# Optimization experiments

Hardware: AMD Instinct MI355X
Metric: run time of the kernel (lower is better)

## Reference

```python
import jax, jax.numpy as jnp
import numpy as np

B, N, E = 2, 16384, 262144          # batch, nodes, directed edges (avg deg 16)
K, D, Wm = 256, 3, 1                # nmodes, ndims, nmeasures
C, L, FC = 128, 4, 128              # channels, Fourier layers, fc hidden
IN_DIM, OUT_DIM = 3, 1


def setup_inputs() -> dict:
    key = jax.random.key(0)
    ks = jax.random.split(key, 20)
    s = 1.0 / (C * C)
    inp = {
        "x": jax.random.normal(ks[0], (B, N, IN_DIM), jnp.float32),
        "nodes": jax.random.uniform(ks[1], (B, N, D), jnp.float32),
        "node_mask": jnp.ones((B, N, 1), jnp.float32),
        "node_weights": jax.random.uniform(ks[2], (B, N, Wm), jnp.float32) / N,
        "directed_edges": jax.random.randint(ks[3], (B, E, 2), 0, N),
        "edge_gradient_weights": jax.random.normal(ks[4], (B, E, D), jnp.float32),
        "modes": jax.random.normal(ks[5], (K, D, Wm), jnp.float32),
        "sp_L": jnp.ones((D, Wm), jnp.float32),
        "weights_c": s * jax.random.uniform(ks[6], (L, C, C, K, Wm), jnp.float32),
        "weights_s": s * jax.random.uniform(ks[7], (L, C, C, K, Wm), jnp.float32),
        "weights_0": s * jax.random.uniform(ks[8], (L, C, C, 1, Wm), jnp.float32),
        "fc0_w": jax.random.normal(ks[9], (C, IN_DIM), jnp.float32) * 0.1,
        "fc0_b": jnp.zeros((C,), jnp.float32),
        "ws_w": jax.random.normal(ks[10], (L, C, C), jnp.float32) * 0.05,
        "ws_b": jnp.zeros((L, C), jnp.float32),
        "gws_w": jax.random.normal(ks[11], (L, C, D * C), jnp.float32) * 0.05,
        "gws_b": jnp.zeros((L, C), jnp.float32),
        "fc1_w": jax.random.normal(ks[12], (FC, C), jnp.float32) * 0.05,
        "fc1_b": jnp.zeros((FC,), jnp.float32),
        "fc2_w": jax.random.normal(ks[13], (OUT_DIM, FC), jnp.float32) * 0.05,
        "fc2_b": jnp.zeros((OUT_DIM,), jnp.float32),
    }
    return inp


def _gelu(x):
    return jax.nn.gelu(x, approximate=False)  # torch F.gelu default = exact erf


def _compute_gradient(f, directed_edges, edge_gradient_weights):
    # f: [B, C, N] -> gradients [B, C*D, N] via directed-edge scatter-add
    fT = jnp.transpose(f, (0, 2, 1))                       # [B, N, C]
    tgt, src = directed_edges[..., 0], directed_edges[..., 1]
    f_src = jnp.take_along_axis(fT, src[..., None], axis=1)  # [B, E, C]
    f_tgt = jnp.take_along_axis(fT, tgt[..., None], axis=1)
    msg = jnp.einsum('bed,bec->becd', edge_gradient_weights, f_src - f_tgt)
    msg = msg.reshape(msg.shape[0], msg.shape[1], -1)        # [B, E, C*D]

    def scat(m, t):
        return jnp.zeros((fT.shape[1], m.shape[-1]), m.dtype).at[t].add(m)

    g = jax.vmap(scat)(msg, tgt)                             # [B, N, C*D]
    return jnp.transpose(g, (0, 2, 1))


def _spectral_conv(x, wc, wsn, w0, bc, bs, b0, wbc, wbs, wb0):
    # x: [B, C_in, N]
    xc = jnp.einsum('bix,bxkw->bikw', x, wbc)
    xs = -jnp.einsum('bix,bxkw->bikw', x, wbs)
    x0 = jnp.einsum('bix,bxkw->bikw', x, wb0)
    fc = jnp.einsum('bikw,iokw->bokw', xc, wc) - jnp.einsum('bikw,iokw->bokw', xs, wsn)
    fs = jnp.einsum('bikw,iokw->bokw', xs, wc) + jnp.einsum('bikw,iokw->bokw', xc, wsn)
    f0 = jnp.einsum('bikw,iokw->bokw', x0, w0)
    return (jnp.einsum('bokw,bxkw->box', f0, b0)
            + 2.0 * jnp.einsum('bokw,bxkw->box', fc, bc)
            - 2.0 * jnp.einsum('bokw,bxkw->box', fs, bs))


def reference(x, nodes, node_mask, node_weights, directed_edges, edge_gradient_weights,
              modes, sp_L, weights_c, weights_s, weights_0,
              fc0_w, fc0_b, ws_w, ws_b, gws_w, gws_b, fc1_w, fc1_b, fc2_w, fc2_b):
    # Fourier bases with learnable length-scale sp_L: [K,D,Wm]*[D,Wm]
    temp = jnp.einsum('bxd,kdw->bxkw', nodes, modes * sp_L)   # [B,N,K,Wm]
    bc, bs = jnp.cos(temp), jnp.sin(temp)
    b0 = jnp.zeros((temp.shape[0], temp.shape[1], 1, temp.shape[3]), temp.dtype)
    nw = (node_weights * node_mask)[:, :, None, :]            # [B,N,1,Wm]
    wbc, wbs, wb0 = bc * nw, bs * nw, b0 * nw

    h = jnp.einsum('bxi,ci->bxc', x, fc0_w) + fc0_b           # lift [B,N,C]
    h = jnp.transpose(h, (0, 2, 1))                           # [B,C,N]

    for i in range(L):
        x1 = _spectral_conv(h, weights_c[i], weights_s[i], weights_0[i],
                            bc, bs, b0, wbc, wbs, wb0)
        x2 = jnp.einsum('oc,bcn->bon', ws_w[i], h) + ws_b[i][None, :, None]
        grad = _compute_gradient(h, directed_edges, edge_gradient_weights)
        x3 = jnp.einsum('og,bgn->bon', gws_w[i], grad) + gws_b[i][None, :, None]
        h = x1 + x2 + x3
        if i != L - 1:
            h = _gelu(h)

    h = jnp.transpose(h, (0, 2, 1))                           # [B,N,C]
    h = _gelu(jnp.einsum('bnc,fc->bnf', h, fc1_w) + fc1_b)
    out = jnp.einsum('bnf,of->bno', h, fc2_w) + fc2_b         # [B,N,out_dim]
    return out
```

## Files before the change

kernel.cpp:

```cpp
#include <hip/hip_runtime.h>
#include <math.h>

#define Bn 2
#define Nn 16384
#define En 262144
#define Kn 256
#define Cn 128
#define Rn 512
#define Ln 4
#define LDP 72
#define NSPLIT 64

typedef float f32x4 __attribute__((ext_vector_type(4)));
typedef short s16x8 __attribute__((ext_vector_type(8)));

__device__ __forceinline__ float gelu_f(float x){
  return 0.5f*x*(1.0f + erff(x*0.70710678118654752440f));
}
__device__ __forceinline__ unsigned short f2b(float x){
  unsigned int u = __float_as_uint(x);
  unsigned int r = (u + 0x7FFFu + ((u>>16)&1u)) >> 16;
  return (unsigned short)r;
}
__device__ __forceinline__ float b2f(unsigned short h){
  return __uint_as_float(((unsigned int)h)<<16);
}
__device__ __forceinline__ unsigned int pack2(float lo, float hi){
  return (unsigned int)f2b(lo) | ((unsigned int)f2b(hi) << 16);
}


__global__ __launch_bounds__(256) void k_nw(const float* __restrict__ nwt,
                                            const float* __restrict__ msk,
                                            float* __restrict__ nw){
  int i = blockIdx.x*256 + threadIdx.x;
  nw[i] = nwt[i]*msk[i];
}

__global__ __launch_bounds__(256) void k_basis(const float* __restrict__ nodes,
                                               const float* __restrict__ modes,
                                               const float* __restrict__ spl,
                                               unsigned short* __restrict__ basis,
                                               unsigned short* __restrict__ basisT){
  __shared__ unsigned short tile[32*520];
  int gn0 = blockIdx.x*32;
  int tid = threadIdx.x;
  float m0 = modes[tid*3+0]*spl[0];
  float m1 = modes[tid*3+1]*spl[1];
  float m2 = modes[tid*3+2]*spl[2];
  for (int j=0;j<32;j++){
    const float* nd = nodes + (size_t)(gn0+j)*3;
    float t = nd[0]*m0 + nd[1]*m1 + nd[2]*m2;
    float s,c;
    sincosf(t,&s,&c);
    tile[j*520 + tid]       = f2b(c);
    tile[j*520 + 256 + tid] = f2b(s);
  }
  __syncthreads();
  int row = tid>>3, col0 = (tid&7)*64;
  #pragma unroll
  for (int q=0;q<8;q++){
    s16x8 v = *(const s16x8*)&tile[row*520 + col0 + q*8];
    *(s16x8*)(basis + (size_t)(gn0+row)*Rn + col0 + q*8) = v;
  }
  int b = gn0 >> 14;
  int nl = gn0 & (Nn-1);
  #pragma unroll
  for (int h=0; h<2; h++){
    int r = h*256 + tid;
    unsigned short* dst = basisT + ((size_t)(b*Rn + r))*Nn + nl;
    #pragma unroll
    for (int q=0;q<4;q++){
      unsigned short tmp[8];
      #pragma unroll
      for (int e=0;e<8;e++) tmp[e] = tile[(q*8+e)*520 + r];
      *(s16x8*)(dst + q*8) = *(const s16x8*)tmp;
    }
  }
}

__global__ __launch_bounds__(256) void k_lift(const float* __restrict__ x,
                                              const float* __restrict__ w,
                                              const float* __restrict__ bias,
                                              const float* __restrict__ nw,
                                              unsigned short* __restrict__ hg,
                                              unsigned short* __restrict__ hwT){
  __shared__ float ht[64*132];
  int gn0 = blockIdx.x*64;
  int tid = threadIdx.x;
  int c = tid & 127, rh = tid >> 7;
  float w0 = w[c*3], w1 = w[c*3+1], w2 = w[c*3+2], bb = bias[c];
  for (int j=0;j<32;j++){
    int n = rh*32 + j;
    const float* xp = x + (size_t)(gn0+n)*3;
    float v = bb + xp[0]*w0 + xp[1]*w1 + xp[2]*w2;
    ht[n*132 + c] = v;
    hg[(size_t)(gn0+n)*Rn + c] = f2b(v);
  }
  __syncthreads();
  int b = gn0 >> 14, nl = gn0 & (Nn-1);
  int cc = tid>>1, hf = tid&1;
  unsigned short* dst = hwT + ((size_t)(b*Cn + cc))*Nn + nl + hf*32;
  #pragma unroll
  for (int q=0;q<8;q++){
    int n = hf*32 + q*4;
    float4 nv = *(const float4*)&nw[(size_t)b*Nn + nl + n];
    ushort4 pk;
    pk.x = f2b(ht[(n+0)*132+cc]*nv.x);
    pk.y = f2b(ht[(n+1)*132+cc]*nv.y);
    pk.z = f2b(ht[(n+2)*132+cc]*nv.z);
    pk.w = f2b(ht[(n+3)*132+cc]*nv.w);
    *(ushort4*)(dst + q*4) = pk;
  }
}

__global__ __launch_bounds__(128) void k_w2c(const float* __restrict__ ws_w,
                                             const float* __restrict__ ws_b,
                                             const float* __restrict__ gws_w,
                                             const float* __restrict__ gws_b,
                                             unsigned short* __restrict__ W2,
                                             float* __restrict__ bias2){
  int bid = blockIdx.x;
  int tid = threadIdx.x;
  unsigned short* wrow = W2 + (size_t)bid*Rn;
  wrow[tid] = f2b(ws_w[(size_t)bid*Cn + tid]);
  const float* g = gws_w + (size_t)bid*384;
  wrow[128+tid] = f2b(g[tid*3+0]);
  wrow[256+tid] = f2b(g[tid*3+1]);
  wrow[384+tid] = f2b(g[tid*3+2]);
  if (tid==0) bias2[bid] = ws_b[bid] + gws_b[bid];
}

__global__ __launch_bounds__(256) void k_cvt(const float* __restrict__ in,
                                             unsigned short* __restrict__ out, int n){
  int i = blockIdx.x*256 + threadIdx.x;
  if (i < n) out[i] = f2b(in[i]);
}


__global__ __launch_bounds__(256) void k_count(const int* __restrict__ de,
                                               int* __restrict__ cnt){
  int i = blockIdx.x*256 + threadIdx.x;
  int b = i >> 18;
  int tgt = de[(size_t)i*2];
  atomicAdd(&cnt[b*Nn + tgt], 1);
}

__global__ __launch_bounds__(1024) void k_scan(const int* __restrict__ cnt,
                                               int* __restrict__ rowptr,
                                               int* __restrict__ cursor){
  __shared__ int part[1024];
  int t = threadIdx.x;
  int b = t >> 9;
  int li = t & 511;
  int loc[32];
  int s = 0;
  int base = b*Nn + li*32;
  #pragma unroll
  for (int j=0;j<32;j++){ loc[j] = s; s += cnt[base+j]; }
  part[t] = s;
  __syncthreads();
  int run = s;
  for (int off=1; off<512; off<<=1){
    int v = (li >= off) ? part[t-off] : 0;
    __syncthreads();
    part[t] += v;
    __syncthreads();
  }
  int incl = part[t];
  int excl = incl - run;
  int rbase = b*(Nn+1) + li*32;
  #pragma unroll
  for (int j=0;j<32;j++){
    int val = excl + loc[j];
    rowptr[rbase+j] = val;
    cursor[base+j]  = val;
  }
  if (li == 511) rowptr[b*(Nn+1) + Nn] = incl;
}

__global__ __launch_bounds__(256) void k_fill(const int* __restrict__ de,
                                              const float* __restrict__ egw,
                                              int* __restrict__ cursor,
                                              float4* __restrict__ epack){
  int i = blockIdx.x*256 + threadIdx.x;
  int b = i >> 18;
  int tgt = de[(size_t)i*2];
  int src = de[(size_t)i*2+1];
  int pos = atomicAdd(&cursor[b*Nn + tgt], 1);
  const float* g = egw + (size_t)i*3;
  float4 pk;
  pk.x = __int_as_float(src);
  pk.y = g[0]; pk.z = g[1]; pk.w = g[2];
  epack[(size_t)b*En + pos] = pk;
}

__global__ __launch_bounds__(128) void k_grad(const unsigned short* __restrict__ hg_r,
                                              const float4* __restrict__ epack,
                                              const int* __restrict__ rowptr,
                                              unsigned short* __restrict__ hg_w){
  int bid = blockIdx.x;
  int b = bid >> 14, n = bid & (Nn-1);
  int tid = threadIdx.x;
  int wv = tid >> 6;
  int l  = tid & 63;
  const unsigned short* hb = hg_r + (size_t)b*Nn*Rn;
  unsigned int ft2 = *(const unsigned int*)(hb + (size_t)n*Rn + 2*l);
  float ftlo = b2f((unsigned short)(ft2 & 0xffffu));
  float fthi = b2f((unsigned short)(ft2 >> 16));
  int beg = rowptr[b*(Nn+1) + n];
  int end = rowptr[b*(Nn+1) + n + 1];
  const float4* ep = epack + (size_t)b*En;
  float a0lo=0.f,a0hi=0.f,a1lo=0.f,a1hi=0.f,a2lo=0.f,a2hi=0.f;
  int j = beg + wv;
  for (; j + 2 < end; j += 4){
    float4 pk0 = ep[j];
    float4 pk1 = ep[j+2];
    int s0 = __float_as_int(pk0.x);
    int s1 = __float_as_int(pk1.x);
    unsigned int h0 = *(const unsigned int*)(hb + (size_t)s0*Rn + 2*l);
    unsigned int h1 = *(const unsigned int*)(hb + (size_t)s1*Rn + 2*l);
    float d0lo = b2f((unsigned short)(h0 & 0xffffu)) - ftlo;
    float d0hi = b2f((unsigned short)(h0 >> 16))     - fthi;
    float d1lo = b2f((unsigned short)(h1 & 0xffffu)) - ftlo;
    float d1hi = b2f((unsigned short)(h1 >> 16))     - fthi;
    a0lo += pk0.y*d0lo + pk1.y*d1lo;  a0hi += pk0.y*d0hi + pk1.y*d1hi;
    a1lo += pk0.z*d0lo + pk1.z*d1lo;  a1hi += pk0.z*d0hi + pk1.z*d1hi;
    a2lo += pk0.w*d0lo + pk1.w*d1lo;  a2hi += pk0.w*d0hi + pk1.w*d1hi;
  }
  if (j < end){
    float4 pk = ep[j];
    int src = __float_as_int(pk.x);
    unsigned int hv = *(const unsigned int*)(hb + (size_t)src*Rn + 2*l);
    float dlo = b2f((unsigned short)(hv & 0xffffu)) - ftlo;
    float dhi = b2f((unsigned short)(hv >> 16))     - fthi;
    a0lo += pk.y*dlo; a0hi += pk.y*dhi;
    a1lo += pk.z*dlo; a1hi += pk.z*dhi;
    a2lo += pk.w*dlo; a2hi += pk.w*dhi;
  }
  __shared__ float red[64*7];
  if (wv == 1){
    float* r = &red[l*7];
    r[0]=a0lo; r[1]=a0hi; r[2]=a1lo; r[3]=a1hi; r[4]=a2lo; r[5]=a2hi;
  }
  __syncthreads();
  if (wv == 0){
    const float* r = &red[l*7];
    a0lo+=r[0]; a0hi+=r[1]; a1lo+=r[2]; a1hi+=r[3]; a2lo+=r[4]; a2hi+=r[5];
    unsigned short* o = hg_w + (size_t)bid*Rn + Cn;
    *(unsigned int*)(o + 2*l)       = pack2(a0lo, a0hi);
    *(unsigned int*)(o + 128 + 2*l) = pack2(a1lo, a1hi);
    *(unsigned int*)(o + 256 + 2*l) = pack2(a2lo, a2hi);
  }
}

__device__ __forceinline__ void stage_tile(const unsigned short* __restrict__ g, size_t ldg,
                                           unsigned short* __restrict__ lds, int tid){
  int row = tid >> 3;
  int seg = (tid & 7) * 8;
  #pragma unroll
  for (int rb=0; rb<4; rb++){
    s16x8 v = *(const s16x8*)(g + (size_t)(row + rb*32)*ldg + seg);
    *(s16x8*)(lds + (size_t)(row + rb*32)*LDP + seg) = v;
  }
}

__device__ __forceinline__ void mfma_chunk(const unsigned short* __restrict__ As,
                                           const unsigned short* __restrict__ Bs,
                                           f32x4 acc[4][4], int wm, int wn, int lr, int lg){
  #pragma unroll
  for (int kk=0; kk<2; kk++){
    s16x8 a[4], b[4];
    #pragma unroll
    for (int i=0;i<4;i++)
      a[i] = *(const s16x8*)(As + (size_t)(wm*64 + i*16 + lr)*LDP + kk*32 + lg*8);
    #pragma unroll
    for (int i=0;i<4;i++)
      b[i] = *(const s16x8*)(Bs + (size_t)(wn*64 + i*16 + lr)*LDP + kk*32 + lg*8);
    #pragma unroll
    for (int i=0;i<4;i++)
      #pragma unroll
      for (int j=0;j<4;j++)
        acc[i][j] = __builtin_amdgcn_mfma_f32_16x16x32_bf16(a[i], b[j], acc[i][j], 0, 0, 0);
  }
}

__global__ __launch_bounds__(256) void k_fwd_mfma(const unsigned short* __restrict__ basisT,
                                                  const unsigned short* __restrict__ hwT,
                                                  float* __restrict__ part){
  __shared__ unsigned short As[128*LDP];
  __shared__ unsigned short Bs[128*LDP];
  int tid = threadIdx.x;
  int mt = blockIdx.x;
  int ks = blockIdx.y;
  int b  = blockIdx.z;
  const int KSP = Nn/NSPLIT;
  const unsigned short* A  = basisT + ((size_t)(b*Rn + mt*128))*Nn + (size_t)ks*KSP;
  const unsigned short* Bp = hwT   + ((size_t)(b*Cn))*Nn + (size_t)ks*KSP;
  f32x4 acc[4][4] = {};
  int l = tid & 63, w = tid >> 6, wm = w >> 1, wn = w & 1, lr = l & 15, lg = l >> 4;
  for (int k0 = 0; k0 < KSP; k0 += 64){
    stage_tile(A + k0, Nn, As, tid);
    stage_tile(Bp + k0, Nn, Bs, tid);
    __syncthreads();
    mfma_chunk(As, Bs, acc, wm, wn, lr, lg);
    __syncthreads();
  }
  float* pb = part + ((size_t)ks*Bn + b)*(Cn*Rn);
  int r0 = mt*128 + wm*64;
  int c0 = wn*64;
  #pragma unroll
  for (int i=0;i<4;i++)
    #pragma unroll
    for (int j=0;j<4;j++){
      int r = r0 + i*16 + lg*4;
      int c = c0 + j*16 + lr;
      *(f32x4*)&pb[(size_t)c*Rn + r] = acc[i][j];
    }
}

__global__ __launch_bounds__(256) void k_reduce(const float* __restrict__ part,
                                                float* __restrict__ xf){
  int idx = blockIdx.x*256 + threadIdx.x;
  float s = 0.f;
  #pragma unroll 8
  for (int ks=0; ks<NSPLIT; ks++)
    s += part[(size_t)ks*(Bn*Cn*Rn) + idx];
  xf[idx] = s;
}

__global__ __launch_bounds__(512) void k_mm(const float* __restrict__ xf,
                                            const float* __restrict__ wc,
                                            const float* __restrict__ ws,
                                            unsigned short* __restrict__ Fbf){
  int o = blockIdx.x;
  int tid = threadIdx.x;
  int half = tid >> 8, t = tid & 255;
  float fc0=0.f, fs0=0.f, fc1=0.f, fs1=0.f;
  for (int ii=0; ii<64; ii++){
    int i = half*64 + ii;
    float wcv = wc[((size_t)i*Cn + o)*Kn + t];
    float wsv = ws[((size_t)i*Cn + o)*Kn + t];
    float x0c = xf[(size_t)i*Rn + t];
    float x0s = xf[(size_t)i*Rn + 256 + t];
    float x1c = xf[(size_t)Cn*Rn + (size_t)i*Rn + t];
    float x1s = xf[(size_t)Cn*Rn + (size_t)i*Rn + 256 + t];
    fc0 += x0c*wcv + x0s*wsv;  fs0 += x0c*wsv - x0s*wcv;
    fc1 += x1c*wcv + x1s*wsv;  fs1 += x1c*wsv - x1s*wcv;
  }
  __shared__ float red[4][256];
  if (half){ red[0][t]=fc0; red[1][t]=fs0; red[2][t]=fc1; red[3][t]=fs1; }
  __syncthreads();
  if (!half){
    fc0 += red[0][t]; fs0 += red[1][t];
    fc1 += red[2][t]; fs1 += red[3][t];
    unsigned short* f0 = Fbf + (size_t)o*Rn;
    unsigned short* f1 = Fbf + (size_t)Cn*Rn + (size_t)o*Rn;
    f0[t]     = f2b( 2.f*fc0);
    f0[256+t] = f2b(-2.f*fs0);
    f1[t]     = f2b( 2.f*fc1);
    f1[256+t] = f2b(-2.f*fs1);
  }
}

template<int GELU, int WRITE_HWT>
__global__ __launch_bounds__(256) void k_invcomb(const unsigned short* __restrict__ basis,
                                                 const unsigned short* __restrict__ Fbf,
                                                 unsigned short* __restrict__ hg,
                                                 const unsigned short* __restrict__ W2l,
                                                 const float* __restrict__ bias2l,
                                                 const float* __restrict__ nw,
                                                 unsigned short* __restrict__ hwT){
  __shared__ unsigned short As[128*LDP];
  __shared__ unsigned short Bs[128*LDP];
  int tid = threadIdx.x;
  int nt = blockIdx.x;
  int b  = blockIdx.y;
  size_t nbase = (size_t)b*Nn + (size_t)nt*128;
  f32x4 acc[4][4] = {};
  int l = tid & 63, w = tid >> 6, wm = w >> 1, wn = w & 1, lr = l & 15, lg = l >> 4;
  const unsigned short* A1 = basis + nbase*Rn;
  const unsigned short* B1 = Fbf + (size_t)b*Cn*Rn;
  for (int k0=0;k0<512;k0+=64){
    stage_tile(A1+k0, Rn, As, tid);
    stage_tile(B1+k0, Rn, Bs, tid);
    __syncthreads();
    mfma_chunk(As,Bs,acc,wm,wn,lr,lg);
    __syncthreads();
  }
  const unsigned short* A2 = hg + nbase*Rn;
  for (int k0=0;k0<512;k0+=64){
    stage_tile(A2+k0, Rn, As, tid);
    stage_tile(W2l+k0, Rn, Bs, tid);
    __syncthreads();
    mfma_chunk(As,Bs,acc,wm,wn,lr,lg);
    __syncthreads();
  }
  int n0 = wm*64, c0 = wn*64;
  #pragma unroll
  for (int i=0;i<4;i++){
    int nloc = n0 + i*16 + lg*4;
    #pragma unroll
    for (int j=0;j<4;j++){
      int c = c0 + j*16 + lr;
      float bsv = bias2l[c];
      float v[4];
      #pragma unroll
      for (int e=0;e<4;e++){
        v[e] = acc[i][j][e] + bsv;
        if (GELU) v[e] = gelu_f(v[e]);
        hg[(nbase + nloc + e)*Rn + c] = f2b(v[e]);
      }
      if (WRITE_HWT){
        float4 w4 = *(const float4*)&nw[(size_t)b*Nn + nt*128 + nloc];
        ushort4 pk;
        pk.x = f2b(v[0]*w4.x); pk.y = f2b(v[1]*w4.y);
        pk.z = f2b(v[2]*w4.z); pk.w = f2b(v[3]*w4.w);
        *(ushort4*)&hwT[((size_t)(b*Cn + c))*Nn + nt*128 + nloc] = pk;
      }
    }
  }
}

__global__ __launch_bounds__(256) void k_fc1(const unsigned short* __restrict__ hg,
                                             const unsigned short* __restrict__ fw,
                                             const float* __restrict__ fb,
                                             unsigned short* __restrict__ h2){
  __shared__ unsigned short As[128*LDP];
  __shared__ unsigned short Bs[128*LDP];
  int tid = threadIdx.x;
  int nt = blockIdx.x;
  int b  = blockIdx.y;
  size_t nbase = (size_t)b*Nn + (size_t)nt*128;
  f32x4 acc[4][4] = {};
  int l = tid & 63, w = tid >> 6, wm = w >> 1, wn = w & 1, lr = l & 15, lg = l >> 4;
  const unsigned short* A = hg + nbase*Rn;
  for (int k0=0;k0<128;k0+=64){
    stage_tile(A+k0, Rn, As, tid);
    stage_tile(fw+k0, Cn, Bs, tid);
    __syncthreads();
    mfma_chunk(As,Bs,acc,wm,wn,lr,lg);
    __syncthreads();
  }
  int n0 = wm*64, c0 = wn*64;
  #pragma unroll
  for (int i=0;i<4;i++){
    int nloc = n0 + i*16 + lg*4;
    #pragma unroll
    for (int j=0;j<4;j++){
      int c = c0 + j*16 + lr;
      float bsv = fb[c];
      #pragma unroll
      for (int e=0;e<4;e++){
        float v = gelu_f(acc[i][j][e] + bsv);
        h2[(nbase + nloc + e)*Cn + c] = f2b(v);
      }
    }
  }
}

__global__ __launch_bounds__(256) void k_out(const unsigned short* __restrict__ h2,
                                             const float* __restrict__ w,
                                             const float* __restrict__ bptr,
                                             float* __restrict__ outp){
  int tid = threadIdx.x;
  int node = blockIdx.x*4 + (tid>>6);
  int f = tid & 63;
  const unsigned short* hp = h2 + (size_t)node*Cn;
  float s = b2f(hp[f])*w[f] + b2f(hp[f+64])*w[f+64];
  #pragma unroll
  for (int off=32; off>0; off>>=1) s += __shfl_down(s, off);
  if (f==0) outp[node] = s + bptr[0];
}

static constexpr size_t OB_BASIS  = 0;
static constexpr size_t OB_BASIST = OB_BASIS  + 33554432;
static constexpr size_t OB_HG     = OB_BASIST + 33554432;
static constexpr size_t OB_HWT    = OB_HG     + 33554432;
static constexpr size_t OB_H2     = OB_HWT    + 8388608;
static constexpr size_t OB_NW     = OB_H2     + 8388608;
static constexpr size_t OB_XF     = OB_NW     + 131072;
static constexpr size_t OB_FBF    = OB_XF     + 524288;
static constexpr size_t OB_W2     = OB_FBF    + 262144;
static constexpr size_t OB_B2     = OB_W2     + 524288;
static constexpr size_t OB_FC1W   = OB_B2     + 2048;
static constexpr size_t OB_EPACK  = OB_FC1W   + 32768;
static constexpr size_t OB_INT    = OB_EPACK  + 8388608;
static constexpr size_t OB_PART   = OB_INT    + 524288;

extern "C" void kernel_launch(void* const* d_in, const int* in_sizes, int n_in,
                              void* d_out, int out_size, void* d_ws, size_t ws_size,
                              hipStream_t stream) {
  const float* x            = (const float*)d_in[0];
  const float* nodes        = (const float*)d_in[1];
  const float* node_mask    = (const float*)d_in[2];
  const float* node_weights = (const float*)d_in[3];
  const int*   de           = (const int*)  d_in[4];
  const float* egw          = (const float*)d_in[5];
  const float* modes        = (const float*)d_in[6];
  const float* spl          = (const float*)d_in[7];
  const float* wc           = (const float*)d_in[8];
  const float* wsp          = (const float*)d_in[9];
  const float* fc0_w        = (const float*)d_in[11];
  const float* fc0_b        = (const float*)d_in[12];
  const float* ws_w         = (const float*)d_in[13];
  const float* ws_b         = (const float*)d_in[14];
  const float* gws_w        = (const float*)d_in[15];
  const float* gws_b        = (const float*)d_in[16];
  const float* fc1_w        = (const float*)d_in[17];
  const float* fc1_b        = (const float*)d_in[18];
  const float* fc2_w        = (const float*)d_in[19];
  const float* fc2_b        = (const float*)d_in[20];
  float* outp = (float*)d_out;

  char* wsb = (char*)d_ws;
  unsigned short* basis  = (unsigned short*)(wsb + OB_BASIS);
  unsigned short* basisT = (unsigned short*)(wsb + OB_BASIST);
  unsigned short* hg     = (unsigned short*)(wsb + OB_HG);
  unsigned short* hwT    = (unsigned short*)(wsb + OB_HWT);
  unsigned short* h2     = (unsigned short*)(wsb + OB_H2);
  float* nw              = (float*)(wsb + OB_NW);
  float* xf              = (float*)(wsb + OB_XF);
  unsigned short* Fbf    = (unsigned short*)(wsb + OB_FBF);
  unsigned short* W2     = (unsigned short*)(wsb + OB_W2);
  float* bias2           = (float*)(wsb + OB_B2);
  unsigned short* fc1wb  = (unsigned short*)(wsb + OB_FC1W);
  float4* epack          = (float4*)(wsb + OB_EPACK);
  int* count  = (int*)(wsb + OB_INT);
  int* rowptr = count + Bn*Nn;
  int* cursor = rowptr + Bn*(Nn+1);
  float* part = (float*)(wsb + OB_PART);

  k_nw<<<(Bn*Nn)/256, 256, 0, stream>>>(node_weights, node_mask, nw);
  k_basis<<<(Bn*Nn)/32, 256, 0, stream>>>(nodes, modes, spl, basis, basisT);
  k_lift<<<(Bn*Nn)/64, 256, 0, stream>>>(x, fc0_w, fc0_b, nw, hg, hwT);

  (void)hipMemsetAsync(count, 0, (size_t)Bn*Nn*sizeof(int), stream);
  k_count<<<(Bn*En)/256, 256, 0, stream>>>(de, count);
  k_scan<<<1, 1024, 0, stream>>>(count, rowptr, cursor);
  k_fill<<<(Bn*En)/256, 256, 0, stream>>>(de, egw, cursor, epack);

  k_w2c<<<Ln*Cn, 128, 0, stream>>>(ws_w, ws_b, gws_w, gws_b, W2, bias2);
  k_cvt<<<64, 256, 0, stream>>>(fc1_w, fc1wb, Cn*Cn);

  for (int l=0; l<Ln; l++){
    k_fwd_mfma<<<dim3(4,NSPLIT,2), 256, 0, stream>>>(basisT, hwT, part);
    k_reduce<<<(Bn*Cn*Rn)/256, 256, 0, stream>>>(part, xf);
    k_mm<<<Cn, 512, 0, stream>>>(xf, wc + (size_t)l*Cn*Cn*Kn,
                                 wsp + (size_t)l*Cn*Cn*Kn, Fbf);
    k_grad<<<Bn*Nn, 128, 0, stream>>>(hg, epack, rowptr, hg);
    if (l < Ln-1){
      k_invcomb<1,1><<<dim3(Nn/128,2), 256, 0, stream>>>(
          basis, Fbf, hg, W2 + (size_t)l*Cn*Rn, bias2 + l*Cn, nw, hwT);
    } else {
      k_invcomb<0,0><<<dim3(Nn/128,2), 256, 0, stream>>>(
          basis, Fbf, hg, W2 + (size_t)l*Cn*Rn, bias2 + l*Cn, nw, hwT);
    }
  }

  k_fc1<<<dim3(Nn/128,2), 256, 0, stream>>>(hg, fc1wb, fc1_b, h2);
  k_out<<<(Bn*Nn)/4, 256, 0, stream>>>(h2, fc2_w, fc2_b, outp);
}
```

Baseline: 562.0 us.

## Gather gradients from compact h copy, split spectral matmul, halve forward split

Adds a compact [N,128] bf16 copy of the hidden state (hpack) that the edge-gradient gather and fc1 read, replacing the old 512-stride rows. Gathered rows become denser and fit cache better. The spectral weight contraction k_mm is split across two input-channel halves for more blocks, and a new small kernel sums the two halves and converts to bf16. NSPLIT in the forward transform drops from 64 to 32, which shrinks the partial-sum reduction but gives fewer blocks. The extra hpack writes and one extra launch per layer are the added cost.

```diff
diff --git a/kernel.cpp b/kernel.cpp
--- a/kernel.cpp
+++ b/kernel.cpp
@@ -9,7 +9,7 @@
 #define Rn 512
 #define Ln 4
 #define LDP 72
-#define NSPLIT 64
+#define NSPLIT 32
 
 typedef float f32x4 __attribute__((ext_vector_type(4)));
 typedef short s16x8 __attribute__((ext_vector_type(8)));
@@ -84,6 +84,7 @@
                                               const float* __restrict__ bias,
                                               const float* __restrict__ nw,
                                               unsigned short* __restrict__ hg,
+                                              unsigned short* __restrict__ hpack,
                                               unsigned short* __restrict__ hwT){
   __shared__ float ht[64*132];
   int gn0 = blockIdx.x*64;
@@ -95,7 +96,9 @@
     const float* xp = x + (size_t)(gn0+n)*3;
     float v = bb + xp[0]*w0 + xp[1]*w1 + xp[2]*w2;
     ht[n*132 + c] = v;
-    hg[(size_t)(gn0+n)*Rn + c] = f2b(v);
+    unsigned short hv = f2b(v);
+    hg[(size_t)(gn0+n)*Rn + c] = hv;
+    hpack[(size_t)(gn0+n)*Cn + c] = hv;
   }
   __syncthreads();
   int b = gn0 >> 14, nl = gn0 & (Nn-1);
@@ -195,7 +198,7 @@
   epack[(size_t)b*En + pos] = pk;
 }
 
-__global__ __launch_bounds__(128) void k_grad(const unsigned short* __restrict__ hg_r,
+__global__ __launch_bounds__(128) void k_grad(const unsigned short* __restrict__ hpack,
                                               const float4* __restrict__ epack,
                                               const int* __restrict__ rowptr,
                                               unsigned short* __restrict__ hg_w){
@@ -204,8 +207,8 @@
   int tid = threadIdx.x;
   int wv = tid >> 6;
   int l  = tid & 63;
-  const unsigned short* hb = hg_r + (size_t)b*Nn*Rn;
-  unsigned int ft2 = *(const unsigned int*)(hb + (size_t)n*Rn + 2*l);
+  const unsigned short* hb = hpack + (size_t)b*Nn*Cn;
+  unsigned int ft2 = *(const unsigned int*)(hb + (size_t)n*Cn + 2*l);
   float ftlo = b2f((unsigned short)(ft2 & 0xffffu));
   float fthi = b2f((unsigned short)(ft2 >> 16));
   int beg = rowptr[b*(Nn+1) + n];
@@ -218,8 +221,8 @@
     float4 pk1 = ep[j+2];
     int s0 = __float_as_int(pk0.x);
     int s1 = __float_as_int(pk1.x);
-    unsigned int h0 = *(const unsigned int*)(hb + (size_t)s0*Rn + 2*l);
-    unsigned int h1 = *(const unsigned int*)(hb + (size_t)s1*Rn + 2*l);
+    unsigned int h0 = *(const unsigned int*)(hb + (size_t)s0*Cn + 2*l);
+    unsigned int h1 = *(const unsigned int*)(hb + (size_t)s1*Cn + 2*l);
     float d0lo = b2f((unsigned short)(h0 & 0xffffu)) - ftlo;
     float d0hi = b2f((unsigned short)(h0 >> 16))     - fthi;
     float d1lo = b2f((unsigned short)(h1 & 0xffffu)) - ftlo;
@@ -231,7 +234,7 @@
   if (j < end){
     float4 pk = ep[j];
     int src = __float_as_int(pk.x);
-    unsigned int hv = *(const unsigned int*)(hb + (size_t)src*Rn + 2*l);
+    unsigned int hv = *(const unsigned int*)(hb + (size_t)src*Cn + 2*l);
     float dlo = b2f((unsigned short)(hv & 0xffffu)) - ftlo;
     float dhi = b2f((unsigned short)(hv >> 16))     - fthi;
     a0lo += pk.y*dlo; a0hi += pk.y*dhi;
@@ -332,13 +335,15 @@
 __global__ __launch_bounds__(512) void k_mm(const float* __restrict__ xf,
                                             const float* __restrict__ wc,
                                             const float* __restrict__ ws,
-                                            unsigned short* __restrict__ Fbf){
-  int o = blockIdx.x;
+                                            float* __restrict__ Fpart){
+  int o  = blockIdx.x;
+  int is = blockIdx.y;
   int tid = threadIdx.x;
   int half = tid >> 8, t = tid & 255;
+  int ibase = is*64 + half*32;
   float fc0=0.f, fs0=0.f, fc1=0.f, fs1=0.f;
-  for (int ii=0; ii<64; ii++){
-    int i = half*64 + ii;
+  for (int ii=0; ii<32; ii++){
+    int i = ibase + ii;
     float wcv = wc[((size_t)i*Cn + o)*Kn + t];
     float wsv = ws[((size_t)i*Cn + o)*Kn + t];
     float x0c = xf[(size_t)i*Rn + t];
@@ -354,22 +359,29 @@
   if (!half){
     fc0 += red[0][t]; fs0 += red[1][t];
     fc1 += red[2][t]; fs1 += red[3][t];
-    unsigned short* f0 = Fbf + (size_t)o*Rn;
-    unsigned short* f1 = Fbf + (size_t)Cn*Rn + (size_t)o*Rn;
-    f0[t]     = f2b( 2.f*fc0);
-    f0[256+t] = f2b(-2.f*fs0);
-    f1[t]     = f2b( 2.f*fc1);
-    f1[256+t] = f2b(-2.f*fs1);
-  }
-}
-
-template<int GELU, int WRITE_HWT>
+    float* f0 = Fpart + ((size_t)(is*Bn + 0)*Cn + o)*Rn;
+    float* f1 = Fpart + ((size_t)(is*Bn + 1)*Cn + o)*Rn;
+    f0[t]     = fc0;  f0[256+t] = fs0;
+    f1[t]     = fc1;  f1[256+t] = fs1;
+  }
+}
+
+__global__ __launch_bounds__(256) void k_fcvt(const float* __restrict__ Fpart,
+                                              unsigned short* __restrict__ Fbf){
+  int idx = blockIdx.x*256 + threadIdx.x;
+  float s = Fpart[idx] + Fpart[idx + Bn*Cn*Rn];
+  float sc = ((idx & 511) < 256) ? 2.f : -2.f;
+  Fbf[idx] = f2b(sc*s);
+}
+
+template<int GELU, int WRITE_AUX>
 __global__ __launch_bounds__(256) void k_invcomb(const unsigned short* __restrict__ basis,
                                                  const unsigned short* __restrict__ Fbf,
                                                  unsigned short* __restrict__ hg,
                                                  const unsigned short* __restrict__ W2l,
                                                  const float* __restrict__ bias2l,
                                                  const float* __restrict__ nw,
+                                                 unsigned short* __restrict__ hpack,
                                                  unsigned short* __restrict__ hwT){
   __shared__ unsigned short As[128*LDP];
   __shared__ unsigned short Bs[128*LDP];
@@ -409,9 +421,11 @@
       for (int e=0;e<4;e++){
         v[e] = acc[i][j][e] + bsv;
         if (GELU) v[e] = gelu_f(v[e]);
-        hg[(nbase + nloc + e)*Rn + c] = f2b(v[e]);
+        unsigned short hv = f2b(v[e]);
+        hpack[(nbase + nloc + e)*Cn + c] = hv;
+        if (WRITE_AUX) hg[(nbase + nloc + e)*Rn + c] = hv;
       }
-      if (WRITE_HWT){
+      if (WRITE_AUX){
         float4 w4 = *(const float4*)&nw[(size_t)b*Nn + nt*128 + nloc];
         ushort4 pk;
         pk.x = f2b(v[0]*w4.x); pk.y = f2b(v[1]*w4.y);
@@ -422,7 +436,7 @@
   }
 }
 
-__global__ __launch_bounds__(256) void k_fc1(const unsigned short* __restrict__ hg,
+__global__ __launch_bounds__(256) void k_fc1(const unsigned short* __restrict__ hpack,
                                              const unsigned short* __restrict__ fw,
                                              const float* __restrict__ fb,
                                              unsigned short* __restrict__ h2){
@@ -434,9 +448,9 @@
   size_t nbase = (size_t)b*Nn + (size_t)nt*128;
   f32x4 acc[4][4] = {};
   int l = tid & 63, w = tid >> 6, wm = w >> 1, wn = w & 1, lr = l & 15, lg = l >> 4;
-  const unsigned short* A = hg + nbase*Rn;
+  const unsigned short* A = hpack + nbase*Cn;
   for (int k0=0;k0<128;k0+=64){
-    stage_tile(A+k0, Rn, As, tid);
+    stage_tile(A+k0, Cn, As, tid);
     stage_tile(fw+k0, Cn, Bs, tid);
     __syncthreads();
     mfma_chunk(As,Bs,acc,wm,wn,lr,lg);
@@ -478,10 +492,12 @@
 static constexpr size_t OB_HG     = OB_BASIST + 33554432;
 static constexpr size_t OB_HWT    = OB_HG     + 33554432;
 static constexpr size_t OB_H2     = OB_HWT    + 8388608;
-static constexpr size_t OB_NW     = OB_H2     + 8388608;
+static constexpr size_t OB_HP     = OB_H2     + 8388608;
+static constexpr size_t OB_NW     = OB_HP     + 8388608;
 static constexpr size_t OB_XF     = OB_NW     + 131072;
 static constexpr size_t OB_FBF    = OB_XF     + 524288;
-static constexpr size_t OB_W2     = OB_FBF    + 262144;
+static constexpr size_t OB_FPART  = OB_FBF    + 262144;
+static constexpr size_t OB_W2     = OB_FPART  + 1048576;
 static constexpr size_t OB_B2     = OB_W2     + 524288;
 static constexpr size_t OB_FC1W   = OB_B2     + 2048;
 static constexpr size_t OB_EPACK  = OB_FC1W   + 32768;
@@ -519,9 +535,11 @@
   unsigned short* hg     = (unsigned short*)(wsb + OB_HG);
   unsigned short* hwT    = (unsigned short*)(wsb + OB_HWT);
   unsigned short* h2     = (unsigned short*)(wsb + OB_H2);
+  unsigned short* hpack  = (unsigned short*)(wsb + OB_HP);
   float* nw              = (float*)(wsb + OB_NW);
   float* xf              = (float*)(wsb + OB_XF);
   unsigned short* Fbf    = (unsigned short*)(wsb + OB_FBF);
+  float* Fpart           = (float*)(wsb + OB_FPART);
   unsigned short* W2     = (unsigned short*)(wsb + OB_W2);
   float* bias2           = (float*)(wsb + OB_B2);
   unsigned short* fc1wb  = (unsigned short*)(wsb + OB_FC1W);
@@ -533,7 +551,7 @@
 
   k_nw<<<(Bn*Nn)/256, 256, 0, stream>>>(node_weights, node_mask, nw);
   k_basis<<<(Bn*Nn)/32, 256, 0, stream>>>(nodes, modes, spl, basis, basisT);
-  k_lift<<<(Bn*Nn)/64, 256, 0, stream>>>(x, fc0_w, fc0_b, nw, hg, hwT);
+  k_lift<<<(Bn*Nn)/64, 256, 0, stream>>>(x, fc0_w, fc0_b, nw, hg, hpack, hwT);
 
   (void)hipMemsetAsync(count, 0, (size_t)Bn*Nn*sizeof(int), stream);
   k_count<<<(Bn*En)/256, 256, 0, stream>>>(de, count);
@@ -546,18 +564,19 @@
   for (int l=0; l<Ln; l++){
     k_fwd_mfma<<<dim3(4,NSPLIT,2), 256, 0, stream>>>(basisT, hwT, part);
     k_reduce<<<(Bn*Cn*Rn)/256, 256, 0, stream>>>(part, xf);
-    k_mm<<<Cn, 512, 0, stream>>>(xf, wc + (size_t)l*Cn*Cn*Kn,
-                                 wsp + (size_t)l*Cn*Cn*Kn, Fbf);
-    k_grad<<<Bn*Nn, 128, 0, stream>>>(hg, epack, rowptr, hg);
+    k_mm<<<dim3(Cn,2), 512, 0, stream>>>(xf, wc + (size_t)l*Cn*Cn*Kn,
+                                         wsp + (size_t)l*Cn*Cn*Kn, Fpart);
+    k_fcvt<<<(Bn*Cn*Rn)/256, 256, 0, stream>>>(Fpart, Fbf);
+    k_grad<<<Bn*Nn, 128, 0, stream>>>(hpack, epack, rowptr, hg);
     if (l < Ln-1){
       k_invcomb<1,1><<<dim3(Nn/128,2), 256, 0, stream>>>(
-          basis, Fbf, hg, W2 + (size_t)l*Cn*Rn, bias2 + l*Cn, nw, hwT);
+          basis, Fbf, hg, W2 + (size_t)l*Cn*Rn, bias2 + l*Cn, nw, hpack, hwT);
     } else {
       k_invcomb<0,0><<<dim3(Nn/128,2), 256, 0, stream>>>(
-          basis, Fbf, hg, W2 + (size_t)l*Cn*Rn, bias2 + l*Cn, nw, hwT);
+          basis, Fbf, hg, W2 + (size_t)l*Cn*Rn, bias2 + l*Cn, nw, hpack, hwT);
     }
   }
 
-  k_fc1<<<dim3(Nn/128,2), 256, 0, stream>>>(hg, fc1wb, fc1_b, h2);
+  k_fc1<<<dim3(Nn/128,2), 256, 0, stream>>>(hpack, fc1wb, fc1_b, h2);
   k_out<<<(Bn*Nn)/4, 256, 0, stream>>>(h2, fc2_w, fc2_b, outp);
 }
```

Result: faster. 545.1 us (-3.0%).
